# Optimization experiments

Hardware: AMD Instinct MI355X
Metric: run time of the kernel (lower is better)

The kernel has to match this reference:

```python
import jax, jax.numpy as jnp
import numpy as np

B, S, D = 4, 2048, 512
H, DQK, DV = 6, 64, 64
PROJ = (DQK + DQK + DV) * H  # 1152
EPS = 1e-5


def setup_inputs() -> dict:
    key = jax.random.key(0)
    ks = jax.random.split(key, 5)
    sc = 0.05
    return {
        "x": jax.random.normal(ks[0], (B, S, D), jnp.float32),
        "Wp": jax.random.normal(ks[1], (PROJ, D), jnp.float32) * sc,
        "bp": jax.random.normal(ks[2], (PROJ,), jnp.float32) * sc,
        "Wo": jax.random.normal(ks[3], (D, H * DV), jnp.float32) * sc,
        "bo": jax.random.normal(ks[4], (D,), jnp.float32) * sc,
        "gamma": jnp.ones((D,), jnp.float32),
        "beta": jnp.zeros((D,), jnp.float32),
    }


def reference(x, Wp, bp, Wo, bo, gamma, beta):
    b, s, d = x.shape
    # 1x1 Conv1d projection == pointwise linear: [b,s,d] @ [d,proj] -> [b,s,proj]
    proj = jnp.einsum("bsd,pd->bsp", x, Wp) + bp
    q, k, v = proj[..., : H * DQK], proj[..., H * DQK : 2 * H * DQK], proj[..., 2 * H * DQK :]
    # split heads -> [b,h,s,depth]
    q = q.reshape(b, s, H, DQK).transpose(0, 2, 1, 3)
    k = k.reshape(b, s, H, DQK).transpose(0, 2, 1, 3)
    v = v.reshape(b, s, H, DV).transpose(0, 2, 1, 3)
    scores = jnp.einsum("bhqd,bhkd->bhqk", q, k) / jnp.sqrt(jnp.float32(DQK))
    attn = jax.nn.softmax(scores, axis=-1)  # softmax over kv axis
    out = jnp.einsum("bhqk,bhkd->bhqd", attn, v)
    # concat heads -> [b,s,h*dv]
    concat = out.transpose(0, 2, 1, 3).reshape(b, s, H * DV)
    y = jnp.einsum("bsf,df->bsd", concat, Wo) + bo
    z = x + y
    mu = jnp.mean(z, axis=-1, keepdims=True)
    var = jnp.mean(jnp.square(z - mu), axis=-1, keepdims=True)
    return (z - mu) / jnp.sqrt(var + EPS) * gamma + beta
```

## Files before the change

kernel.cpp:

```cpp
#include <hip/hip_runtime.h>

typedef __bf16 bf16;
typedef __bf16 bf16x8 __attribute__((ext_vector_type(8)));
typedef __bf16 bf16x4 __attribute__((ext_vector_type(4)));
typedef float  f32x4  __attribute__((ext_vector_type(4)));

#define BB 4
#define SS 2048
#define DD 512
#define HH 6
#define DH 64
#define PROJ 1152
#define FF 384
#define LDK 72

__device__ __forceinline__ bool probe_fp32(const unsigned* p) {
    return p[0] == 0x3F800000u;
}

__device__ __forceinline__ float fast_exp2(float x) {
#if __has_builtin(__builtin_amdgcn_exp2f)
    return __builtin_amdgcn_exp2f(x);
#else
    return __expf(x * 0.69314718f);
#endif
}

struct CvtSrcs { const void* s[7]; };

#define CB0 524288
#define CB1 598016
#define CB2 622592
#define CB3 622736
#define CB4 622800
#define CB5 622864
#define CB6 622928

__global__ __launch_bounds__(256) void cvt_all_kernel(
    CvtSrcs srcs, bf16* __restrict__ dst, const unsigned* __restrict__ probe)
{
    const int t = blockIdx.x * 256 + threadIdx.x;
    if (t >= CB6) return;
    int seg, base;
    if      (t < CB0) { seg = 0; base = 0;   }
    else if (t < CB1) { seg = 1; base = CB0; }
    else if (t < CB2) { seg = 2; base = CB1; }
    else if (t < CB3) { seg = 3; base = CB2; }
    else if (t < CB4) { seg = 4; base = CB3; }
    else if (t < CB5) { seg = 5; base = CB4; }
    else              { seg = 6; base = CB5; }
    const int li = (t - base) * 8;
    if (probe_fp32(probe)) {
        const float* s = (const float*)srcs.s[seg] + li;
        bf16x8 o;
#pragma unroll
        for (int j = 0; j < 8; ++j) o[j] = (bf16)s[j];
        *(bf16x8*)&dst[(size_t)t * 8] = o;
    } else {
        *(bf16x8*)&dst[(size_t)t * 8] =
            *(const bf16x8*)((const bf16*)srcs.s[seg] + li);
    }
}

template<int MERGE>
__global__ __launch_bounds__(256) void gemm_bt_kernel(
    const bf16* __restrict__ A, const float* __restrict__ lpart,
    const bf16* __restrict__ B, const bf16* __restrict__ bias,
    bf16* __restrict__ Cout, int M, int N, int K)
{
    __shared__ __attribute__((aligned(16))) bf16 sA[64 * LDK];
    __shared__ __attribute__((aligned(16))) bf16 sB[128 * LDK];

    const int tid  = threadIdx.x;
    const int lane = tid & 63;
    const int wave = tid >> 6;
    const int wn = wave * 32;
    const int l15 = lane & 15;
    const int quad = lane >> 4;
    const int bm = blockIdx.x * 64;
    const int bn = blockIdx.y * 128;
    const int KT = K / 64;

    int srowA[2], srowB[4];
    const int scol = (tid & 7) << 3;
#pragma unroll
    for (int j = 0; j < 2; ++j) srowA[j] = (j * 256 + tid) >> 3;
#pragma unroll
    for (int j = 0; j < 4; ++j) srowB[j] = (j * 256 + tid) >> 3;

    const bf16* pA[2]; const bf16* pB[4];
    const float* pl0[2];
#pragma unroll
    for (int j = 0; j < 2; ++j) {
        if (MERGE) {
            int row = bm + srowA[j];
            int b = row >> 11, q = row & (SS - 1);
            pA[j]  = A + ((size_t)(b * HH) * SS + q) * DH + scol;
            pl0[j] = lpart + (size_t)(b * HH) * SS + q;
        } else {
            pA[j] = A + (size_t)(bm + srowA[j]) * K + scol;
        }
    }
#pragma unroll
    for (int j = 0; j < 4; ++j)
        pB[j] = B + (size_t)(bn + srowB[j]) * K + scol;

    bf16x8 arb[2], a1b[2], brb[4];
    float l0[2], l1[2];

    auto loadAB = [&]() {
#pragma unroll
        for (int j = 0; j < 2; ++j) {
            arb[j] = *(const bf16x8*)pA[j];
            if (MERGE) {
                a1b[j] = *(const bf16x8*)(pA[j] + (size_t)BB * HH * SS * DH);
                l0[j] = pl0[j][0];
                l1[j] = pl0[j][(size_t)BB * HH * SS];
                pA[j]  += (size_t)SS * DH;
                pl0[j] += SS;
            } else {
                pA[j] += 64;
            }
        }
#pragma unroll
        for (int j = 0; j < 4; ++j) {
            brb[j] = *(const bf16x8*)pB[j];
            pB[j] += 64;
        }
    };

    loadAB();

    const f32x4 fzero = {0.f, 0.f, 0.f, 0.f};
    f32x4 acc[4][2];
#pragma unroll
    for (int mi = 0; mi < 4; ++mi)
#pragma unroll
        for (int ni = 0; ni < 2; ++ni) acc[mi][ni] = fzero;

    for (int kt = 0; kt < KT; ++kt) {
        __syncthreads();
#pragma unroll
        for (int j = 0; j < 2; ++j) {
            if (MERGE) {
                float inv = 1.f / (l0[j] + l1[j]);
                bf16x8 m;
#pragma unroll
                for (int e = 0; e < 8; ++e)
                    m[e] = (bf16)(((float)arb[j][e] + (float)a1b[j][e]) * inv);
                *(bf16x8*)&sA[srowA[j] * LDK + scol] = m;
            } else {
                *(bf16x8*)&sA[srowA[j] * LDK + scol] = arb[j];
            }
        }
#pragma unroll
        for (int j = 0; j < 4; ++j)
            *(bf16x8*)&sB[srowB[j] * LDK + scol] = brb[j];
        __syncthreads();
        if (kt + 1 < KT) loadAB();

#pragma unroll
        for (int kk = 0; kk < 2; ++kk) {
            bf16x8 af[4], bfr[2];
#pragma unroll
            for (int i = 0; i < 4; ++i)
                af[i] = *(const bf16x8*)&sA[(i * 16 + l15) * LDK + kk * 32 + quad * 8];
#pragma unroll
            for (int i = 0; i < 2; ++i)
                bfr[i] = *(const bf16x8*)&sB[(wn + i * 16 + l15) * LDK + kk * 32 + quad * 8];
#pragma unroll
            for (int mi = 0; mi < 4; ++mi)
#pragma unroll
                for (int ni = 0; ni < 2; ++ni)
                    acc[mi][ni] = __builtin_amdgcn_mfma_f32_16x16x32_bf16(
                        af[mi], bfr[ni], acc[mi][ni], 0, 0, 0);
        }
    }

#pragma unroll
    for (int mi = 0; mi < 4; ++mi) {
        int row = bm + mi * 16 + quad * 4;
#pragma unroll
        for (int ni = 0; ni < 2; ++ni) {
            int col = bn + wn + ni * 16 + l15;
            float bv = (float)bias[col];
#pragma unroll
            for (int r = 0; r < 4; ++r)
                Cout[(size_t)(row + r) * N + col] = (bf16)(acc[mi][ni][r] + bv);
        }
    }
}

__global__ __launch_bounds__(256) void vt_kernel(
    const bf16* __restrict__ proj, bf16* __restrict__ Vt)
{
    __shared__ __attribute__((aligned(16))) bf16 lt[64 * LDK];

    const int tid = threadIdx.x;
    const int s0 = blockIdx.x * 64;
    const int bh = blockIdx.y;
    const int b = bh / HH, h = bh % HH;

#pragma unroll
    for (int i = 0; i < 2; ++i) {
        int vid = i * 256 + tid;
        int sl = vid >> 3;
        int dc = (vid & 7) << 3;
        bf16x8 v = *(const bf16x8*)&proj[
            (size_t)(b * SS + s0 + sl) * PROJ + 2 * HH * DH + h * DH + dc];
#pragma unroll
        for (int j = 0; j < 8; ++j) {
            int d = dc + j;
            lt[d * LDK + (sl ^ (((d >> 3) & 3) * 8))] = v[j];
        }
    }
    __syncthreads();

#pragma unroll
    for (int i = 0; i < 2; ++i) {
        int vid = i * 256 + tid;
        int d = vid >> 3;
        int sc = (vid & 7) << 3;
        bf16x8 v = *(const bf16x8*)&lt[d * LDK + (sc ^ (((d >> 3) & 3) * 8))];
        *(bf16x8*)&Vt[(size_t)bh * DH * SS + (size_t)d * SS + s0 + sc] = v;
    }
}

__global__ __launch_bounds__(256) void attn_kernel(
    const bf16* __restrict__ proj, const bf16* __restrict__ Vt,
    bf16* __restrict__ Opart, float* __restrict__ lpart)
{
    __shared__ __attribute__((aligned(16))) bf16 sK [64 * 64];
    __shared__ __attribute__((aligned(16))) bf16 sVt[64 * 64];
    __shared__ __attribute__((aligned(16))) bf16 sP [4 * 32 * 64];

    const int tid  = threadIdx.x;
    const int lane = tid & 63;
    const int wave = tid >> 6;
    const int l15  = lane & 15;
    const int quad = lane >> 4;

    const int bh = blockIdx.y;
    const int b = bh / HH, h = bh % HH;
    const int q0 = blockIdx.x * 128;
    const int kz = blockIdx.z;
    const bf16* base = proj + (size_t)b * SS * PROJ;
    const bf16* vtb  = Vt + (size_t)bh * DH * SS;

    const int sr = tid >> 3;
    const int sc = (tid & 7) << 3;

    const float QS = 0.18033688f;
    bf16x8 qf[2][2];
#pragma unroll
    for (int g = 0; g < 2; ++g) {
        const int qrow = q0 + wave * 32 + g * 16 + l15;
#pragma unroll
        for (int ks = 0; ks < 2; ++ks) {
            qf[ks][g] = *(const bf16x8*)&base[
                (size_t)qrow * PROJ + h * DH + ks * 32 + quad * 8];
#pragma unroll
            for (int j = 0; j < 8; ++j)
                qf[ks][g][j] = (bf16)((float)qf[ks][g][j] * QS);
        }
    }

    const f32x4 fzero = {0.f, 0.f, 0.f, 0.f};
    f32x4 lacc[2] = {fzero, fzero};
    f32x4 oacc[2][4];
#pragma unroll
    for (int g = 0; g < 2; ++g)
#pragma unroll
        for (int fi = 0; fi < 4; ++fi) oacc[g][fi] = fzero;

    bf16* pw = &sP[wave * 32 * 64];

    const int kt0 = kz * (SS / 128);
    const int kt1 = kt0 + SS / 128;

    const bf16* pk[2]; const bf16* pv[2];
#pragma unroll
    for (int i = 0; i < 2; ++i) {
        int r = i * 32 + sr;
        pk[i] = &base[(size_t)(kt0 * 64 + r) * PROJ + HH * DH + h * DH + sc];
        pv[i] = &vtb[(size_t)r * SS + kt0 * 64 + sc];
    }
    auto loadKV = [&](bf16x8 (&kr)[2], bf16x8 (&vr)[2]) {
#pragma unroll
        for (int i = 0; i < 2; ++i) {
            kr[i] = *(const bf16x8*)pk[i];
            vr[i] = *(const bf16x8*)pv[i];
            pk[i] += (size_t)64 * PROJ;
            pv[i] += 64;
        }
    };

    bf16x8 kA[2], vA[2], kB[2], vB[2];
    loadKV(kA, vA);
    loadKV(kB, vB);

    auto tile = [&](int kt, bf16x8 (&kr)[2], bf16x8 (&vr)[2]) {
        __syncthreads();
#pragma unroll
        for (int i = 0; i < 2; ++i) {
            int r = i * 32 + sr;
            const int swc = sc ^ ((r & 7) << 3);
            *(bf16x8*)&sK [r * 64 + swc] = kr[i];
            *(bf16x8*)&sVt[r * 64 + swc] = vr[i];
        }
        __syncthreads();
        if (kt + 2 < kt1) loadKV(kr, vr);

        f32x4 st[2][4];
#pragma unroll
        for (int mi = 0; mi < 4; ++mi) {
            const int row = mi * 16 + l15;
            const int sw = (row & 7) << 3;
            bf16x8 af0 = *(const bf16x8*)&sK[row * 64 + ((quad * 8) ^ sw)];
            bf16x8 af1 = *(const bf16x8*)&sK[row * 64 + ((32 + quad * 8) ^ sw)];
            __builtin_amdgcn_s_setprio(1);
#pragma unroll
            for (int g = 0; g < 2; ++g) {
                st[g][mi] = __builtin_amdgcn_mfma_f32_16x16x32_bf16(
                    af0, qf[0][g], fzero, 0, 0, 0);
                st[g][mi] = __builtin_amdgcn_mfma_f32_16x16x32_bf16(
                    af1, qf[1][g], st[g][mi], 0, 0, 0);
            }
            __builtin_amdgcn_s_setprio(0);
        }

#pragma unroll
        for (int g = 0; g < 2; ++g)
#pragma unroll
            for (int mi = 0; mi < 4; ++mi) {
#pragma unroll
                for (int r = 0; r < 4; ++r)
                    st[g][mi][r] = fast_exp2(st[g][mi][r]);
                lacc[g] += st[g][mi];
            }

#pragma unroll
        for (int g = 0; g < 2; ++g) {
            const int r = g * 16 + l15;
            const int sw = (r & 7) << 3;
#pragma unroll
            for (int mi = 0; mi < 4; ++mi) {
                bf16x4 p4;
#pragma unroll
                for (int e = 0; e < 4; ++e) p4[e] = (bf16)st[g][mi][e];
                *(bf16x4*)&pw[r * 64 + ((mi * 16 + quad * 4) ^ sw)] = p4;
            }
        }

#pragma unroll
        for (int ks = 0; ks < 2; ++ks) {
            bf16x8 bfrag[2];
#pragma unroll
            for (int g = 0; g < 2; ++g) {
                const int r = g * 16 + l15;
                bfrag[g] = *(const bf16x8*)&pw[
                    r * 64 + ((ks * 32 + quad * 8) ^ ((r & 7) << 3))];
            }
#pragma unroll
            for (int fi = 0; fi < 4; ++fi) {
                const int row = fi * 16 + l15;
                bf16x8 af = *(const bf16x8*)&sVt[
                    row * 64 + ((ks * 32 + quad * 8) ^ ((row & 7) << 3))];
                __builtin_amdgcn_s_setprio(1);
#pragma unroll
                for (int g = 0; g < 2; ++g)
                    oacc[g][fi] = __builtin_amdgcn_mfma_f32_16x16x32_bf16(
                        af, bfrag[g], oacc[g][fi], 0, 0, 0);
                __builtin_amdgcn_s_setprio(0);
            }
        }
    };

    for (int kt = kt0; kt < kt1; kt += 2) {
        tile(kt,     kA, vA);
        tile(kt + 1, kB, vB);
    }

    float l_part[2];
#pragma unroll
    for (int g = 0; g < 2; ++g) {
        l_part[g] = lacc[g][0] + lacc[g][1] + lacc[g][2] + lacc[g][3];
        l_part[g] += __shfl_xor(l_part[g], 16);
        l_part[g] += __shfl_xor(l_part[g], 32);
    }

    const size_t zoff = (size_t)(kz * BB * HH + bh) * SS;
#pragma unroll
    for (int g = 0; g < 2; ++g) {
        const int qg = q0 + wave * 32 + g * 16 + l15;
        bf16* orow = Opart + (zoff + qg) * DH;
#pragma unroll
        for (int fi = 0; fi < 4; ++fi) {
            bf16x4 o4;
#pragma unroll
            for (int r = 0; r < 4; ++r) o4[r] = (bf16)oacc[g][fi][r];
            *(bf16x4*)&orow[fi * 16 + quad * 4] = o4;
        }
    }
    if (lane < 16) {
#pragma unroll
        for (int g = 0; g < 2; ++g)
            lpart[zoff + q0 + wave * 32 + g * 16 + lane] = l_part[g];
    }
}

__global__ __launch_bounds__(256) void ln_kernel(
    const bf16* __restrict__ x, const bf16* __restrict__ y,
    const bf16* __restrict__ gamma, const bf16* __restrict__ beta,
    void* __restrict__ out, const unsigned* __restrict__ probe)
{
    const bool f32 = probe_fp32(probe);
    const int lane = threadIdx.x & 63;
    const int wave = threadIdx.x >> 6;
    const int row = blockIdx.x * 4 + wave;
    const size_t off = (size_t)row * DD + lane * 8;

    bf16x8 xv = *(const bf16x8*)&x[off];
    bf16x8 yv = *(const bf16x8*)&y[off];
    float z[8];
    float s = 0.f;
#pragma unroll
    for (int j = 0; j < 8; ++j) { z[j] = (float)xv[j] + (float)yv[j]; s += z[j]; }
#pragma unroll
    for (int m = 1; m < 64; m <<= 1) s += __shfl_xor(s, m);
    float mu = s * (1.f / DD);
    float s2 = 0.f;
#pragma unroll
    for (int j = 0; j < 8; ++j) { float d = z[j] - mu; s2 += d * d; }
#pragma unroll
    for (int m = 1; m < 64; m <<= 1) s2 += __shfl_xor(s2, m);
    float rs = rsqrtf(s2 * (1.f / DD) + 1e-5f);

    bf16x8 gm = *(const bf16x8*)&gamma[lane * 8];
    bf16x8 be = *(const bf16x8*)&beta[lane * 8];
    if (f32) {
        f32x4 o0, o1;
#pragma unroll
        for (int j = 0; j < 4; ++j) {
            o0[j] = (z[j]     - mu) * rs * (float)gm[j]     + (float)be[j];
            o1[j] = (z[j + 4] - mu) * rs * (float)gm[j + 4] + (float)be[j + 4];
        }
        *(f32x4*)&((float*)out)[off]     = o0;
        *(f32x4*)&((float*)out)[off + 4] = o1;
    } else {
        bf16x8 o;
#pragma unroll
        for (int j = 0; j < 8; ++j)
            o[j] = (bf16)((z[j] - mu) * rs * (float)gm[j] + (float)be[j]);
        *(bf16x8*)&((bf16*)out)[off] = o;
    }
}

extern "C" void kernel_launch(void* const* d_in, const int* in_sizes, int n_in,
                              void* d_out, int out_size, void* d_ws, size_t ws_size,
                              hipStream_t stream)
{
    const unsigned* probe = (const unsigned*)d_in[5];

    char* ws = (char*)d_ws;
    size_t o = 0;
    bf16* xb   = (bf16*)(ws + o); o += (size_t)BB * SS * DD * 2;
    bf16* Wpb  = (bf16*)(ws + o); o += (size_t)PROJ * DD * 2;
    bf16* Wob  = (bf16*)(ws + o); o += (size_t)DD * FF * 2;
    bf16* bpb  = (bf16*)(ws + o); o += PROJ * 2;
    bf16* bob  = (bf16*)(ws + o); o += DD * 2;
    bf16* gb   = (bf16*)(ws + o); o += DD * 2;
    bf16* bb   = (bf16*)(ws + o); o += DD * 2;
    bf16* proj   = (bf16*)(ws + o); o += (size_t)BB * SS * PROJ * 2;
    bf16* vtbuf  = (bf16*)(ws + o); o += (size_t)BB * HH * DH * SS * 2;
    bf16* Opart  = (bf16*)(ws + o); o += (size_t)2 * BB * HH * SS * DH * 2;
    float* lpart = (float*)(ws + o); o += (size_t)2 * BB * HH * SS * 4;
    bf16* ybuf = proj;

    CvtSrcs srcs;
    srcs.s[0] = d_in[0]; srcs.s[1] = d_in[1]; srcs.s[2] = d_in[3];
    srcs.s[3] = d_in[2]; srcs.s[4] = d_in[4]; srcs.s[5] = d_in[5];
    srcs.s[6] = d_in[6];
    cvt_all_kernel<<<(CB6 + 255) / 256, 256, 0, stream>>>(srcs, xb, probe);

    gemm_bt_kernel<0><<<dim3((BB * SS) / 64, PROJ / 128), 256, 0, stream>>>(
        xb, nullptr, Wpb, bpb, proj, BB * SS, PROJ, DD);
    vt_kernel<<<dim3(SS / 64, BB * HH), 256, 0, stream>>>(proj, vtbuf);
    attn_kernel<<<dim3(SS / 128, BB * HH, 2), 256, 0, stream>>>(
        proj, vtbuf, Opart, lpart);
    gemm_bt_kernel<1><<<dim3((BB * SS) / 64, DD / 128), 256, 0, stream>>>(
        Opart, lpart, Wob, bob, ybuf, BB * SS, DD, FF);
    ln_kernel<<<dim3((BB * SS) / 4), 256, 0, stream>>>(
        xb, ybuf, gb, bb, d_out, probe);
}
```

Before: 162.1 us.

## Double-buffer K/V tiles in LDS with one barrier per iteration

The attention kernel's K and V^T shared-memory tiles become double buffers. Each iteration writes the next tile into the alternate buffer while computing on the current one, so the two __syncthreads per tile drop to one. Register prefetch also goes from two tiles in flight to one. This doubles LDS use for K/V, which may lower occupancy, and leaves less global-load latency hidden by the register prefetch.

```diff
diff --git a/kernel.cpp b/kernel.cpp
--- a/kernel.cpp
+++ b/kernel.cpp
@@ -230,8 +230,8 @@
     const bf16* __restrict__ proj, const bf16* __restrict__ Vt,
     bf16* __restrict__ Opart, float* __restrict__ lpart)
 {
-    __shared__ __attribute__((aligned(16))) bf16 sK [64 * 64];
-    __shared__ __attribute__((aligned(16))) bf16 sVt[64 * 64];
+    __shared__ __attribute__((aligned(16))) bf16 sK [2][64 * 64];
+    __shared__ __attribute__((aligned(16))) bf16 sVt[2][64 * 64];
     __shared__ __attribute__((aligned(16))) bf16 sP [4 * 32 * 64];
 
     const int tid  = threadIdx.x;
@@ -285,7 +285,9 @@
         pk[i] = &base[(size_t)(kt0 * 64 + r) * PROJ + HH * DH + h * DH + sc];
         pv[i] = &vtb[(size_t)r * SS + kt0 * 64 + sc];
     }
-    auto loadKV = [&](bf16x8 (&kr)[2], bf16x8 (&vr)[2]) {
+
+    bf16x8 kr[2], vr[2];
+    auto loadKV = [&]() {
 #pragma unroll
         for (int i = 0; i < 2; ++i) {
             kr[i] = *(const bf16x8*)pk[i];
@@ -294,30 +296,35 @@
             pv[i] += 64;
         }
     };
-
-    bf16x8 kA[2], vA[2], kB[2], vB[2];
-    loadKV(kA, vA);
-    loadKV(kB, vB);
-
-    auto tile = [&](int kt, bf16x8 (&kr)[2], bf16x8 (&vr)[2]) {
-        __syncthreads();
+    auto stage = [&](int buf) {
 #pragma unroll
         for (int i = 0; i < 2; ++i) {
             int r = i * 32 + sr;
             const int swc = sc ^ ((r & 7) << 3);
-            *(bf16x8*)&sK [r * 64 + swc] = kr[i];
-            *(bf16x8*)&sVt[r * 64 + swc] = vr[i];
-        }
+            *(bf16x8*)&sK [buf][r * 64 + swc] = kr[i];
+            *(bf16x8*)&sVt[buf][r * 64 + swc] = vr[i];
+        }
+    };
+
+    loadKV();
+    stage(0);
+    loadKV();
+
+    for (int t = kt0; t < kt1; ++t) {
+        const int cur = t & 1;
         __syncthreads();
-        if (kt + 2 < kt1) loadKV(kr, vr);
+        if (t + 1 < kt1) {
+            stage(cur ^ 1);
+            if (t + 2 < kt1) loadKV();
+        }
 
         f32x4 st[2][4];
 #pragma unroll
         for (int mi = 0; mi < 4; ++mi) {
             const int row = mi * 16 + l15;
             const int sw = (row & 7) << 3;
-            bf16x8 af0 = *(const bf16x8*)&sK[row * 64 + ((quad * 8) ^ sw)];
-            bf16x8 af1 = *(const bf16x8*)&sK[row * 64 + ((32 + quad * 8) ^ sw)];
+            bf16x8 af0 = *(const bf16x8*)&sK[cur][row * 64 + ((quad * 8) ^ sw)];
+            bf16x8 af1 = *(const bf16x8*)&sK[cur][row * 64 + ((32 + quad * 8) ^ sw)];
             __builtin_amdgcn_s_setprio(1);
 #pragma unroll
             for (int g = 0; g < 2; ++g) {
@@ -364,7 +371,7 @@
 #pragma unroll
             for (int fi = 0; fi < 4; ++fi) {
                 const int row = fi * 16 + l15;
-                bf16x8 af = *(const bf16x8*)&sVt[
+                bf16x8 af = *(const bf16x8*)&sVt[cur][
                     row * 64 + ((ks * 32 + quad * 8) ^ ((row & 7) << 3))];
                 __builtin_amdgcn_s_setprio(1);
 #pragma unroll
@@ -374,11 +381,6 @@
                 __builtin_amdgcn_s_setprio(0);
             }
         }
-    };
-
-    for (int kt = kt0; kt < kt1; kt += 2) {
-        tile(kt,     kA, vA);
-        tile(kt + 1, kB, vB);
     }
 
     float l_part[2];
```

After: 155.7 us. 4.0% less time.
